# Optimization experiments

Hardware: AMD Instinct MI355X
Metric: run time of the kernel (lower is better)

## Reference

```python
import jax, jax.numpy as jnp
import numpy as np

N_NODES = 50000
N_EDGES = 600000
N_GRAPHS = 64
HID = 128
NLAYERS = 4
IN_DIM = 5
NCLS = 5
EPS = 1e-5


def setup_inputs() -> dict:
    key = jax.random.key(0)
    ks = jax.random.split(key, 16)
    x = jax.random.normal(ks[0], (N_NODES, IN_DIM), dtype=jnp.float32)
    edge_index = jax.random.randint(ks[1], (2, N_EDGES), 0, N_NODES, dtype=jnp.int64)
    batch = jnp.sort(jax.random.randint(ks[2], (N_NODES,), 0, N_GRAPHS, dtype=jnp.int64))
    s = 0.05
    Wp = jax.random.normal(ks[3], (IN_DIM, HID), jnp.float32) * s
    bp = jnp.zeros((HID,), jnp.float32)
    Wg = jax.random.normal(ks[4], (NLAYERS, HID, HID), jnp.float32) * s
    bg = jnp.zeros((NLAYERS, HID), jnp.float32)
    gamma = jnp.ones((NLAYERS, HID), jnp.float32)
    beta = jnp.zeros((NLAYERS, HID), jnp.float32)
    W1 = jax.random.normal(ks[5], (2 * HID, HID), jnp.float32) * s
    b1 = jnp.zeros((HID,), jnp.float32)
    W2 = jax.random.normal(ks[6], (HID, HID // 2), jnp.float32) * s
    b2 = jnp.zeros((HID // 2,), jnp.float32)
    W3 = jax.random.normal(ks[7], (HID // 2, NCLS), jnp.float32) * s
    b3 = jnp.zeros((NCLS,), jnp.float32)
    return {"x": x, "edge_index": edge_index, "batch": batch, "Wp": Wp, "bp": bp,
            "Wg": Wg, "bg": bg, "gamma": gamma, "beta": beta,
            "W1": W1, "b1": b1, "W2": W2, "b2": b2, "W3": W3, "b3": b3}


def reference(x, edge_index, batch, Wp, bp, Wg, bg, gamma, beta, W1, b1, W2, b2, W3, b3):
    N = x.shape[0]
    # GCN with added self-loops and symmetric normalization (PyG GCNConv defaults)
    loop = jnp.arange(N)
    src = jnp.concatenate([edge_index[0], loop])
    dst = jnp.concatenate([edge_index[1], loop])
    deg = jax.ops.segment_sum(jnp.ones_like(dst, dtype=x.dtype), dst, num_segments=N)
    dinv = jax.lax.rsqrt(deg)  # deg >= 1 thanks to self-loops
    norm = dinv[src] * dinv[dst]  # [E+N]
    h = x @ Wp + bp  # [N, HID]
    for i in range(NLAYERS):
        m = h @ Wg[i]
        agg = jax.ops.segment_sum(m[src] * norm[:, None], dst, num_segments=N) + bg[i]
        # BatchNorm1d (training-mode stats over nodes)
        mu = jnp.mean(agg, axis=0)
        var = jnp.var(agg, axis=0)
        h = gamma[i] * (agg - mu) * jax.lax.rsqrt(var + EPS) + beta[i]
        h = jax.nn.relu(h)  # dropout is identity in eval mode
    # mean_max global pooling per graph
    cnt = jax.ops.segment_sum(jnp.ones((N,), h.dtype), batch, num_segments=N_GRAPHS)
    x_mean = jax.ops.segment_sum(h, batch, num_segments=N_GRAPHS) / jnp.maximum(cnt, 1.0)[:, None]
    x_max = jax.ops.segment_max(h, batch, num_segments=N_GRAPHS)
    x_max = jnp.where(jnp.isfinite(x_max), x_max, 0.0)
    pooled = jnp.concatenate([x_mean, x_max], axis=1)  # [B, 2*HID]
    h1 = jax.nn.relu(pooled @ W1 + b1)
    h2 = jax.nn.relu(h1 @ W2 + b2)
    return h2 @ W3 + b3  # [B, num_classes]
```

## Files before the change

kernel.cpp:

```cpp
#include <hip/hip_runtime.h>
#include <hip/hip_bf16.h>

#define N_NODES 50000
#define N_EDGES 600000
#define N_GRAPHS 64
#define HID 128
#define NLAYERS 4
#define IN_DIM 5
#define NCLS 5
#define EPS 1e-5f
#define SCAN_BLK ((N_NODES + 511) / 512)
#define FILL_BLK ((N_EDGES + 255) / 256)
#define POOL_CHUNKS 16
#define BSLOT 64
#define WS 136

typedef __attribute__((ext_vector_type(8))) short s16x8;
typedef __attribute__((ext_vector_type(4))) float f32x4;

__device__ __forceinline__ unsigned short f2bf(float x) {
    unsigned u = __float_as_uint(x);
    unsigned r = (u + 0x7fffu + ((u >> 16) & 1u)) >> 16;
    return (unsigned short)r;
}
__device__ __forceinline__ float2 bfpair(unsigned u) {
    float2 r;
    r.x = __uint_as_float(u << 16);
    r.y = __uint_as_float(u & 0xffff0000u);
    return r;
}
__device__ __forceinline__ float bf2f(unsigned short s) {
    return __uint_as_float(((unsigned)s) << 16);
}


__global__ void k_count(const int* __restrict__ dst, int* __restrict__ cnt) {
    int i = blockIdx.x * blockDim.x + threadIdx.x;
    if (i < N_EDGES) atomicAdd(&cnt[dst[i]], 1);
}

__global__ void k_scan1(const int* __restrict__ cnt, int* __restrict__ rp, int* __restrict__ bsum) {
    __shared__ int s[512];
    int t = threadIdx.x;
    int i = blockIdx.x * 512 + t;
    int v = (i < N_NODES) ? cnt[i] : 0;
    s[t] = v;
    __syncthreads();
    for (int off = 1; off < 512; off <<= 1) {
        int x = (t >= off) ? s[t - off] : 0;
        __syncthreads();
        s[t] += x;
        __syncthreads();
    }
    if (i < N_NODES) rp[i + 1] = s[t];
    if (t == 511) bsum[blockIdx.x] = s[511];
}

__global__ void k_scan2g(int* __restrict__ bsum, const int* __restrict__ batch,
                         int* __restrict__ gstart) {
    if (blockIdx.x == 0) {
        __shared__ int s[128];
        int t = threadIdx.x;
        int v = (t < SCAN_BLK) ? bsum[t] : 0;
        s[t] = v;
        __syncthreads();
        for (int off = 1; off < 128; off <<= 1) {
            int x = (t >= off) ? s[t - off] : 0;
            __syncthreads();
            s[t] += x;
            __syncthreads();
        }
        if (t < SCAN_BLK) bsum[t] = s[t] - v;
    } else {
        int t = threadIdx.x;
        if (t <= N_GRAPHS) {
            int lo = 0, hi = N_NODES;
            while (lo < hi) {
                int mid = (lo + hi) >> 1;
                if (batch[mid] < t) lo = mid + 1; else hi = mid;
            }
            gstart[t] = lo;
        }
    }
}

__global__ void k_scan3d(int* __restrict__ rp, const int* __restrict__ bsum,
                         const int* __restrict__ cnt, float* __restrict__ dinv) {
    int i = blockIdx.x * 512 + threadIdx.x;
    if (i < N_NODES) {
        rp[i + 1] += bsum[blockIdx.x];
        dinv[i] = rsqrtf((float)(cnt[i] + 1));
    }
    if (i == 0) rp[0] = 0;
}

__global__ void k_fillw(const int* __restrict__ src, const int* __restrict__ dst,
                        const int* __restrict__ rp, int* __restrict__ cursor,
                        int2* __restrict__ cw, const float* __restrict__ dinv,
                        const float* __restrict__ Wg, unsigned short* __restrict__ WtG) {
    int b = blockIdx.x;
    if (b < FILL_BLK) {
        int e = b * 256 + threadIdx.x;
        if (e < N_EDGES) {
            int d = dst[e];
            int pos = atomicAdd(&cursor[d], 1);
            int s = src[e];
            int2 p;
            p.x = s;
            p.y = __float_as_int(dinv[s]);
            cw[rp[d] + pos] = p;
        }
    } else {
        int idx = (b - FILL_BLK) * 256 + threadIdx.x;
        int l = idx >> 14;
        int r = idx & 16383;
        int n = r >> 7, k = r & 127;
        WtG[idx] = f2bf(Wg[l * HID * HID + k * HID + n]);
    }
}


__global__ __launch_bounds__(256, 3) void k_gemmM(const unsigned short* __restrict__ Abf,
                                                  const float* __restrict__ x,
                                                  const float* __restrict__ Wp,
                                                  const float* __restrict__ bp,
                                                  const unsigned short* __restrict__ WtG,
                                                  unsigned short* __restrict__ Bm,
                                                  const float* __restrict__ psum,
                                                  const float* __restrict__ psq,
                                                  const float* __restrict__ gamma,
                                                  const float* __restrict__ beta,
                                                  int layer0) {
    __shared__ unsigned short Wt[HID * WS];
    __shared__ unsigned short Al[64 * WS];
    __shared__ float scl[HID], shf[HID];
    int t = threadIdx.x;
    {
        const uint4* Wg4 = (const uint4*)WtG;
        for (int idx = t; idx < HID * 16; idx += 256) {
            int n = idx >> 4, c = idx & 15;
            *(uint4*)&Wt[n * WS + c * 8] = Wg4[idx];
        }
    }
    if (!layer0 && t < HID) {
        float s = 0.f, s2 = 0.f;
#pragma unroll 8
        for (int b = 0; b < BSLOT; b++) {
            s += psum[b * HID + t];
            s2 += psq[b * HID + t];
        }
        const float invN = 1.f / (float)N_NODES;
        float mu = s * invN;
        float var = s2 * invN - mu * mu;
        float rs = rsqrtf(var + EPS) * gamma[t];
        scl[t] = rs;
        shf[t] = beta[t] - mu * rs;
    }
    int lane = t & 63, wv = t >> 6;
    int rbase = (wv & 1) * 32;
    int cbase = (wv >> 1) * 64;
    int mr = lane & 15, q = lane >> 4;
    const int numTiles = (N_NODES + 63) / 64;
    for (int tile = blockIdx.x; tile < numTiles; tile += gridDim.x) {
        int n0 = tile * 64;
        int limRow = min(64, N_NODES - n0);
        __syncthreads();
        if (layer0) {
            for (int idx = t; idx < 64 * HID; idx += 256) {
                int n = idx >> 7, k = idx & 127;
                int node = n0 + n;
                float acc = 0.f;
                if (node < N_NODES) {
                    acc = bp[k];
#pragma unroll
                    for (int j = 0; j < IN_DIM; j++) acc += x[node * IN_DIM + j] * Wp[j * HID + k];
                }
                Al[n * WS + k] = f2bf(acc);
            }
        } else {
            const uint2* Ag = (const uint2*)(Abf + (size_t)n0 * HID);
            for (int idx = t; idx < 64 * 32; idx += 256) {
                int row = idx >> 5, c4 = idx & 31;
                uint2 u = (row < limRow) ? Ag[row * 32 + c4] : make_uint2(0u, 0u);
                float2 ab = bfpair(u.x);
                float2 cd = bfpair(u.y);
                int kf = c4 * 4;
                float4 sc = *(const float4*)&scl[kf];
                float4 sh = *(const float4*)&shf[kf];
                float v0 = fmaxf(ab.x * sc.x + sh.x, 0.f);
                float v1 = fmaxf(ab.y * sc.y + sh.y, 0.f);
                float v2 = fmaxf(cd.x * sc.z + sh.z, 0.f);
                float v3 = fmaxf(cd.y * sc.w + sh.w, 0.f);
                unsigned lo = (unsigned)f2bf(v0) | ((unsigned)f2bf(v1) << 16);
                unsigned hi = (unsigned)f2bf(v2) | ((unsigned)f2bf(v3) << 16);
                *(uint2*)&Al[row * WS + kf] = make_uint2(lo, hi);
            }
        }
        __syncthreads();
        f32x4 acc[2][4];
#pragma unroll
        for (int rt = 0; rt < 2; rt++)
#pragma unroll
            for (int ct = 0; ct < 4; ct++) acc[rt][ct] = (f32x4){0.f, 0.f, 0.f, 0.f};
#pragma unroll
        for (int kk = 0; kk < HID; kk += 32) {
            s16x8 a0 = *(const s16x8*)&Al[(rbase + mr) * WS + kk + q * 8];
            s16x8 a1 = *(const s16x8*)&Al[(rbase + 16 + mr) * WS + kk + q * 8];
#pragma unroll
            for (int ct = 0; ct < 4; ct++) {
                s16x8 b = *(const s16x8*)&Wt[(cbase + ct * 16 + mr) * WS + kk + q * 8];
                acc[0][ct] = __builtin_amdgcn_mfma_f32_16x16x32_bf16(a0, b, acc[0][ct], 0, 0, 0);
                acc[1][ct] = __builtin_amdgcn_mfma_f32_16x16x32_bf16(a1, b, acc[1][ct], 0, 0, 0);
            }
        }
        __syncthreads();
#pragma unroll
        for (int rt = 0; rt < 2; rt++)
#pragma unroll
            for (int ct = 0; ct < 4; ct++)
#pragma unroll
                for (int r = 0; r < 4; r++) {
                    int rloc = rbase + rt * 16 + q * 4 + r;
                    int f = cbase + ct * 16 + mr;
                    Al[rloc * WS + f] = f2bf(acc[rt][ct][r]);
                }
        __syncthreads();
        for (int idx = t; idx < 64 * 16; idx += 256) {
            int row = idx >> 4, c = idx & 15;
            if (row < limRow)
                *(uint4*)&Bm[(size_t)(n0 + row) * HID + c * 8] = *(const uint4*)&Al[row * WS + c * 8];
        }
    }
}


__global__ __launch_bounds__(256) void k_gather(const uint4* __restrict__ Bm4,
                                                const int* __restrict__ rp,
                                                const int2* __restrict__ cw,
                                                const float* __restrict__ dinv,
                                                const float* __restrict__ bg,
                                                unsigned short* __restrict__ Aout,
                                                float* __restrict__ psum,
                                                float* __restrict__ psq) {
    __shared__ float ls[4 * HID], lq[4 * HID];
    int wave = threadIdx.x >> 6;
    int lane = threadIdx.x & 63;
    int s = lane & 15;
    int p = lane >> 4;
    int f = s * 8;
    int v = blockIdx.x * 16 + wave * 4 + p;
    int beg = rp[v], end = rp[v + 1];
    float dv = dinv[v];
    float a0, a1, a2, a3, a4, a5, a6, a7;
    {
        uint4 u = Bm4[(size_t)v * 16 + s];
        float2 q0 = bfpair(u.x), q1 = bfpair(u.y), q2 = bfpair(u.z), q3 = bfpair(u.w);
        a0 = q0.x * dv; a1 = q0.y * dv; a2 = q1.x * dv; a3 = q1.y * dv;
        a4 = q2.x * dv; a5 = q2.y * dv; a6 = q3.x * dv; a7 = q3.y * dv;
    }
    int e = beg;
    for (; e + 1 < end; e += 2) {
        int2 pe0 = cw[e];
        int2 pe1 = cw[e + 1];
        uint4 u0 = Bm4[(size_t)pe0.x * 16 + s];
        uint4 u1 = Bm4[(size_t)pe1.x * 16 + s];
        float w0 = __int_as_float(pe0.y);
        float w1 = __int_as_float(pe1.y);
        float2 x0 = bfpair(u0.x), x1 = bfpair(u0.y), x2 = bfpair(u0.z), x3 = bfpair(u0.w);
        float2 y0 = bfpair(u1.x), y1 = bfpair(u1.y), y2 = bfpair(u1.z), y3 = bfpair(u1.w);
        a0 += x0.x * w0 + y0.x * w1;
        a1 += x0.y * w0 + y0.y * w1;
        a2 += x1.x * w0 + y1.x * w1;
        a3 += x1.y * w0 + y1.y * w1;
        a4 += x2.x * w0 + y2.x * w1;
        a5 += x2.y * w0 + y2.y * w1;
        a6 += x3.x * w0 + y3.x * w1;
        a7 += x3.y * w0 + y3.y * w1;
    }
    if (e < end) {
        int2 pe = cw[e];
        uint4 u = Bm4[(size_t)pe.x * 16 + s];
        float w = __int_as_float(pe.y);
        float2 x0 = bfpair(u.x), x1 = bfpair(u.y), x2 = bfpair(u.z), x3 = bfpair(u.w);
        a0 += x0.x * w; a1 += x0.y * w; a2 += x1.x * w; a3 += x1.y * w;
        a4 += x2.x * w; a5 += x2.y * w; a6 += x3.x * w; a7 += x3.y * w;
    }
    float r0 = a0 * dv + bg[f + 0];
    float r1 = a1 * dv + bg[f + 1];
    float r2 = a2 * dv + bg[f + 2];
    float r3 = a3 * dv + bg[f + 3];
    float r4 = a4 * dv + bg[f + 4];
    float r5 = a5 * dv + bg[f + 5];
    float r6 = a6 * dv + bg[f + 6];
    float r7 = a7 * dv + bg[f + 7];
    unsigned short b0 = f2bf(r0), b1 = f2bf(r1), b2 = f2bf(r2), b3 = f2bf(r3);
    unsigned short b4 = f2bf(r4), b5 = f2bf(r5), b6 = f2bf(r6), b7 = f2bf(r7);
    uint4 o;
    o.x = (unsigned)b0 | ((unsigned)b1 << 16);
    o.y = (unsigned)b2 | ((unsigned)b3 << 16);
    o.z = (unsigned)b4 | ((unsigned)b5 << 16);
    o.w = (unsigned)b6 | ((unsigned)b7 << 16);
    *(uint4*)&Aout[(size_t)v * HID + f] = o;
    float v0 = bf2f(b0), v1 = bf2f(b1), v2 = bf2f(b2), v3 = bf2f(b3);
    float v4 = bf2f(b4), v5 = bf2f(b5), v6 = bf2f(b6), v7 = bf2f(b7);
    float ts0 = v0, ts1 = v1, ts2 = v2, ts3 = v3;
    float ts4 = v4, ts5 = v5, ts6 = v6, ts7 = v7;
    float tq0 = v0 * v0, tq1 = v1 * v1, tq2 = v2 * v2, tq3 = v3 * v3;
    float tq4 = v4 * v4, tq5 = v5 * v5, tq6 = v6 * v6, tq7 = v7 * v7;
    ts0 += __shfl_xor(ts0, 16); ts1 += __shfl_xor(ts1, 16);
    ts2 += __shfl_xor(ts2, 16); ts3 += __shfl_xor(ts3, 16);
    ts4 += __shfl_xor(ts4, 16); ts5 += __shfl_xor(ts5, 16);
    ts6 += __shfl_xor(ts6, 16); ts7 += __shfl_xor(ts7, 16);
    tq0 += __shfl_xor(tq0, 16); tq1 += __shfl_xor(tq1, 16);
    tq2 += __shfl_xor(tq2, 16); tq3 += __shfl_xor(tq3, 16);
    tq4 += __shfl_xor(tq4, 16); tq5 += __shfl_xor(tq5, 16);
    tq6 += __shfl_xor(tq6, 16); tq7 += __shfl_xor(tq7, 16);
    ts0 += __shfl_xor(ts0, 32); ts1 += __shfl_xor(ts1, 32);
    ts2 += __shfl_xor(ts2, 32); ts3 += __shfl_xor(ts3, 32);
    ts4 += __shfl_xor(ts4, 32); ts5 += __shfl_xor(ts5, 32);
    ts6 += __shfl_xor(ts6, 32); ts7 += __shfl_xor(ts7, 32);
    tq0 += __shfl_xor(tq0, 32); tq1 += __shfl_xor(tq1, 32);
    tq2 += __shfl_xor(tq2, 32); tq3 += __shfl_xor(tq3, 32);
    tq4 += __shfl_xor(tq4, 32); tq5 += __shfl_xor(tq5, 32);
    tq6 += __shfl_xor(tq6, 32); tq7 += __shfl_xor(tq7, 32);
    if (p == 0) {
        float* lsw = &ls[wave * HID + f];
        float* lqw = &lq[wave * HID + f];
        lsw[0] = ts0; lsw[1] = ts1; lsw[2] = ts2; lsw[3] = ts3;
        lsw[4] = ts4; lsw[5] = ts5; lsw[6] = ts6; lsw[7] = ts7;
        lqw[0] = tq0; lqw[1] = tq1; lqw[2] = tq2; lqw[3] = tq3;
        lqw[4] = tq4; lqw[5] = tq5; lqw[6] = tq6; lqw[7] = tq7;
    }
    __syncthreads();
    int tt = threadIdx.x;
    if (tt < HID) {
        float ssum = ls[tt] + ls[HID + tt] + ls[2 * HID + tt] + ls[3 * HID + tt];
        float ssq = lq[tt] + lq[HID + tt] + lq[2 * HID + tt] + lq[3 * HID + tt];
        int slot = blockIdx.x & (BSLOT - 1);
        atomicAdd(&psum[slot * HID + tt], ssum);
        atomicAdd(&psq[slot * HID + tt], ssq);
    }
}


__global__ __launch_bounds__(128) void k_pool(const unsigned short* __restrict__ A,
                                              const float* __restrict__ psum,
                                              const float* __restrict__ psq,
                                              const float* __restrict__ gamma,
                                              const float* __restrict__ beta,
                                              const int* __restrict__ gstart,
                                              float* __restrict__ poolPart) {
    int g = blockIdx.x;
    int c = blockIdx.y;
    int f = threadIdx.x;
    float s = 0.f, s2 = 0.f;
#pragma unroll 8
    for (int b = 0; b < BSLOT; b++) {
        s += psum[b * HID + f];
        s2 += psq[b * HID + f];
    }
    const float invN = 1.f / (float)N_NODES;
    float mu = s * invN;
    float var = s2 * invN - mu * mu;
    float sc = rsqrtf(var + EPS) * gamma[f];
    float sh = beta[f] - mu * sc;
    int beg = gstart[g], end = gstart[g + 1];
    int len = end - beg;
    int per = (len + POOL_CHUNKS - 1) / POOL_CHUNKS;
    int s0 = beg + c * per;
    int s1 = min(s0 + per, end);
    float sa = 0.f, sb = 0.f, ma = 0.f, mb = 0.f;
    int n = s0;
    for (; n + 1 < s1; n += 2) {
        float v0 = bf2f(A[(size_t)n * HID + f]);
        float v1 = bf2f(A[(size_t)(n + 1) * HID + f]);
        v0 = fmaxf(v0 * sc + sh, 0.f);
        v1 = fmaxf(v1 * sc + sh, 0.f);
        sa += v0; ma = fmaxf(ma, v0);
        sb += v1; mb = fmaxf(mb, v1);
    }
    if (n < s1) {
        float v = fmaxf(bf2f(A[(size_t)n * HID + f]) * sc + sh, 0.f);
        sa += v; ma = fmaxf(ma, v);
    }
    poolPart[((size_t)g * POOL_CHUNKS + c) * 256 + f] = sa + sb;
    poolPart[((size_t)g * POOL_CHUNKS + c) * 256 + 128 + f] = fmaxf(ma, mb);
}


__global__ __launch_bounds__(128) void k_head(const float* __restrict__ poolPart,
                                              const int* __restrict__ gstart,
                                              const float* __restrict__ W1, const float* __restrict__ b1,
                                              const float* __restrict__ W2, const float* __restrict__ b2,
                                              const float* __restrict__ W3, const float* __restrict__ b3,
                                              float* __restrict__ out) {
    __shared__ float pl[2 * HID];
    __shared__ float h1[HID];
    __shared__ float h2[HID / 2];
    int g = blockIdx.x, t = threadIdx.x;
    float cnt = fmaxf((float)(gstart[g + 1] - gstart[g]), 1.f);
    float s = 0.f, mx = 0.f;
#pragma unroll
    for (int c = 0; c < POOL_CHUNKS; c++) {
        const float* p = &poolPart[((size_t)g * POOL_CHUNKS + c) * 256];
        s += p[t];
        mx = fmaxf(mx, p[128 + t]);
    }
    pl[t] = s / cnt;
    pl[HID + t] = mx;
    __syncthreads();
    float acc = b1[t];
    for (int k = 0; k < 2 * HID; k++) acc += pl[k] * W1[k * HID + t];
    h1[t] = fmaxf(acc, 0.f);
    __syncthreads();
    if (t < HID / 2) {
        float a2 = b2[t];
        for (int k = 0; k < HID; k++) a2 += h1[k] * W2[k * (HID / 2) + t];
        h2[t] = fmaxf(a2, 0.f);
    }
    __syncthreads();
    if (t < NCLS) {
        float a3 = b3[t];
        for (int k = 0; k < HID / 2; k++) a3 += h2[k] * W3[k * NCLS + t];
        out[g * NCLS + t] = a3;
    }
}

extern "C" void kernel_launch(void* const* d_in, const int* in_sizes, int n_in,
                              void* d_out, int out_size, void* d_ws, size_t ws_size,
                              hipStream_t stream) {
    const float* x     = (const float*)d_in[0];
    const int*   ei    = (const int*)d_in[1];
    const int*   batch = (const int*)d_in[2];
    const float* Wp    = (const float*)d_in[3];
    const float* bp    = (const float*)d_in[4];
    const float* Wg    = (const float*)d_in[5];
    const float* bg    = (const float*)d_in[6];
    const float* gamma = (const float*)d_in[7];
    const float* beta  = (const float*)d_in[8];
    const float* W1    = (const float*)d_in[9];
    const float* b1    = (const float*)d_in[10];
    const float* W2    = (const float*)d_in[11];
    const float* b2    = (const float*)d_in[12];
    const float* W3    = (const float*)d_in[13];
    const float* b3    = (const float*)d_in[14];
    const int* src = ei;
    const int* dst = ei + N_EDGES;
    float* out = (float*)d_out;

    char* base = (char*)d_ws;
    size_t off = 0;
    auto alloc = [&](size_t bytes) -> void* {
        void* p = base + off;
        off += (bytes + 255) & ~(size_t)255;
        return p;
    };
    int*   counts = (int*)alloc((size_t)N_NODES * 4);
    int*   cursor = (int*)alloc((size_t)N_NODES * 4);
    float* psum   = (float*)alloc((size_t)NLAYERS * BSLOT * HID * 4);
    float* psq    = (float*)alloc((size_t)NLAYERS * BSLOT * HID * 4);
    size_t zeroBytes = off;
    int*   rp      = (int*)alloc((size_t)(N_NODES + 1) * 4);
    int*   bsum    = (int*)alloc(128 * 4);
    int2*  cw      = (int2*)alloc((size_t)N_EDGES * 8);
    float* dinv    = (float*)alloc((size_t)N_NODES * 4);
    int*   gstart  = (int*)alloc((size_t)(N_GRAPHS + 1) * 4);
    float* poolPart= (float*)alloc((size_t)N_GRAPHS * POOL_CHUNKS * 256 * 4);
    unsigned short* WtG = (unsigned short*)alloc((size_t)NLAYERS * HID * HID * 2);
    unsigned short* A = (unsigned short*)alloc((size_t)N_NODES * HID * 2);
    unsigned short* B = (unsigned short*)alloc((size_t)N_NODES * HID * 2);
    (void)ws_size; (void)in_sizes; (void)n_in; (void)out_size;

    hipMemsetAsync(d_ws, 0, zeroBytes, stream);

    k_count<<<(N_EDGES + 255) / 256, 256, 0, stream>>>(dst, counts);
    k_scan1<<<SCAN_BLK, 512, 0, stream>>>(counts, rp, bsum);
    k_scan2g<<<2, 128, 0, stream>>>(bsum, batch, gstart);
    k_scan3d<<<SCAN_BLK, 512, 0, stream>>>(rp, bsum, counts, dinv);
    k_fillw<<<FILL_BLK + (NLAYERS * HID * HID) / 256, 256, 0, stream>>>(
        src, dst, rp, cursor, cw, dinv, Wg, WtG);

    for (int i = 0; i < NLAYERS; i++) {
        int pl = (i == 0) ? 0 : (i - 1);
        k_gemmM<<<768, 256, 0, stream>>>(A, x, Wp, bp, WtG + (size_t)i * HID * HID, B,
                                         psum + (size_t)pl * BSLOT * HID,
                                         psq + (size_t)pl * BSLOT * HID,
                                         gamma + pl * HID, beta + pl * HID,
                                         (i == 0) ? 1 : 0);
        k_gather<<<N_NODES / 16, 256, 0, stream>>>((const uint4*)B, rp, cw, dinv,
                                                   bg + i * HID, A,
                                                   psum + (size_t)i * BSLOT * HID,
                                                   psq + (size_t)i * BSLOT * HID);
    }
    dim3 pg(N_GRAPHS, POOL_CHUNKS);
    k_pool<<<pg, 128, 0, stream>>>(A, psum + (size_t)3 * BSLOT * HID,
                                   psq + (size_t)3 * BSLOT * HID,
                                   gamma + 3 * HID, beta + 3 * HID, gstart, poolPart);
    k_head<<<N_GRAPHS, 128, 0, stream>>>(poolPart, gstart, W1, b1, W2, b2, W3, b3, out);
}
```

Measured before the change: 379.1 us.

## Merge graph build and all layers into two persistent cooperative kernels with grid barriers

Folds the count/scan/fill preprocessing into one cooperative kernel, and the per-layer GEMM, gather, pooling and head into a second persistent kernel. Separate launches are replaced by a software grid barrier built on atomic counters. The goal is to remove about a dozen kernel launches and their inter-kernel gaps. In exchange, every phase now runs at a fixed grid size with barrier spin overhead. The non-cooperative fallback launch relies on all blocks being co-resident, so it could deadlock.

```diff
diff --git a/kernel.cpp b/kernel.cpp
--- a/kernel.cpp
+++ b/kernel.cpp
@@ -10,10 +10,12 @@
 #define NCLS 5
 #define EPS 1e-5f
 #define SCAN_BLK ((N_NODES + 511) / 512)
-#define FILL_BLK ((N_EDGES + 255) / 256)
 #define POOL_CHUNKS 16
 #define BSLOT 64
 #define WS 136
+#define NT_BUILD (SCAN_BLK * 512)
+#define LGRID 768
+#define LGRID_FB 512
 
 typedef __attribute__((ext_vector_type(8))) short s16x8;
 typedef __attribute__((ext_vector_type(4))) float f32x4;
@@ -33,34 +35,64 @@
     return __uint_as_float(((unsigned)s) << 16);
 }
 
-
-__global__ void k_count(const int* __restrict__ dst, int* __restrict__ cnt) {
-    int i = blockIdx.x * blockDim.x + threadIdx.x;
-    if (i < N_EDGES) atomicAdd(&cnt[dst[i]], 1);
-}
-
-__global__ void k_scan1(const int* __restrict__ cnt, int* __restrict__ rp, int* __restrict__ bsum) {
+__device__ __forceinline__ void gridbar(int* cnt, int* gen, int nblk) {
+    __syncthreads();
+    if (threadIdx.x == 0) {
+        int g = __hip_atomic_load(gen, __ATOMIC_RELAXED, __HIP_MEMORY_SCOPE_AGENT);
+        __threadfence();
+        int a = __hip_atomic_fetch_add(cnt, 1, __ATOMIC_RELAXED, __HIP_MEMORY_SCOPE_AGENT);
+        if (a == nblk - 1) {
+            __hip_atomic_store(cnt, 0, __ATOMIC_RELAXED, __HIP_MEMORY_SCOPE_AGENT);
+            __hip_atomic_store(gen, g + 1, __ATOMIC_RELEASE, __HIP_MEMORY_SCOPE_AGENT);
+        } else {
+            while (__hip_atomic_load(gen, __ATOMIC_RELAXED, __HIP_MEMORY_SCOPE_AGENT) == g)
+                __builtin_amdgcn_s_sleep(2);
+        }
+        __threadfence();
+    }
+    __syncthreads();
+}
+
+
+__global__ __launch_bounds__(512) void k_build(const int* __restrict__ src,
+                                               const int* __restrict__ dst,
+                                               const int* __restrict__ batch,
+                                               const float* __restrict__ Wg,
+                                               int* __restrict__ counts,
+                                               int* __restrict__ cursor,
+                                               float* __restrict__ psum,
+                                               float* __restrict__ psq,
+                                               int* __restrict__ rp,
+                                               int* __restrict__ bsum,
+                                               int2* __restrict__ cw,
+                                               float* __restrict__ dinv,
+                                               int* __restrict__ gstart,
+                                               unsigned short* __restrict__ WtG,
+                                               int* bcnt, int* bgen) {
     __shared__ int s[512];
     int t = threadIdx.x;
-    int i = blockIdx.x * 512 + t;
-    int v = (i < N_NODES) ? cnt[i] : 0;
-    s[t] = v;
-    __syncthreads();
-    for (int off = 1; off < 512; off <<= 1) {
-        int x = (t >= off) ? s[t - off] : 0;
+    int b = blockIdx.x;
+    int gtid = b * 512 + t;
+    for (int i = gtid; i < N_NODES; i += NT_BUILD) { counts[i] = 0; cursor[i] = 0; }
+    for (int i = gtid; i < NLAYERS * BSLOT * HID; i += NT_BUILD) { psum[i] = 0.f; psq[i] = 0.f; }
+    gridbar(bcnt, bgen, SCAN_BLK);
+    for (int e = gtid; e < N_EDGES; e += NT_BUILD) atomicAdd(&counts[dst[e]], 1);
+    gridbar(bcnt, bgen, SCAN_BLK);
+    {
+        int v = (gtid < N_NODES) ? counts[gtid] : 0;
+        s[t] = v;
         __syncthreads();
-        s[t] += x;
-        __syncthreads();
-    }
-    if (i < N_NODES) rp[i + 1] = s[t];
-    if (t == 511) bsum[blockIdx.x] = s[511];
-}
-
-__global__ void k_scan2g(int* __restrict__ bsum, const int* __restrict__ batch,
-                         int* __restrict__ gstart) {
-    if (blockIdx.x == 0) {
-        __shared__ int s[128];
-        int t = threadIdx.x;
+        for (int off = 1; off < 512; off <<= 1) {
+            int x = (t >= off) ? s[t - off] : 0;
+            __syncthreads();
+            s[t] += x;
+            __syncthreads();
+        }
+        if (gtid < N_NODES) rp[gtid + 1] = s[t];
+        if (t == 511) bsum[b] = s[511];
+    }
+    gridbar(bcnt, bgen, SCAN_BLK);
+    if (b == 0) {
         int v = (t < SCAN_BLK) ? bsum[t] : 0;
         s[t] = v;
         __syncthreads();
@@ -71,8 +103,7 @@
             __syncthreads();
         }
         if (t < SCAN_BLK) bsum[t] = s[t] - v;
-    } else {
-        int t = threadIdx.x;
+    } else if (b == 1) {
         if (t <= N_GRAPHS) {
             int lo = 0, hi = N_NODES;
             while (lo < hi) {
@@ -82,36 +113,23 @@
             gstart[t] = lo;
         }
     }
-}
-
-__global__ void k_scan3d(int* __restrict__ rp, const int* __restrict__ bsum,
-                         const int* __restrict__ cnt, float* __restrict__ dinv) {
-    int i = blockIdx.x * 512 + threadIdx.x;
-    if (i < N_NODES) {
-        rp[i + 1] += bsum[blockIdx.x];
-        dinv[i] = rsqrtf((float)(cnt[i] + 1));
-    }
-    if (i == 0) rp[0] = 0;
-}
-
-__global__ void k_fillw(const int* __restrict__ src, const int* __restrict__ dst,
-                        const int* __restrict__ rp, int* __restrict__ cursor,
-                        int2* __restrict__ cw, const float* __restrict__ dinv,
-                        const float* __restrict__ Wg, unsigned short* __restrict__ WtG) {
-    int b = blockIdx.x;
-    if (b < FILL_BLK) {
-        int e = b * 256 + threadIdx.x;
-        if (e < N_EDGES) {
-            int d = dst[e];
-            int pos = atomicAdd(&cursor[d], 1);
-            int s = src[e];
-            int2 p;
-            p.x = s;
-            p.y = __float_as_int(dinv[s]);
-            cw[rp[d] + pos] = p;
-        }
-    } else {
-        int idx = (b - FILL_BLK) * 256 + threadIdx.x;
+    gridbar(bcnt, bgen, SCAN_BLK);
+    if (gtid < N_NODES) {
+        rp[gtid + 1] += bsum[b];
+        dinv[gtid] = rsqrtf((float)(counts[gtid] + 1));
+    }
+    if (gtid == 0) rp[0] = 0;
+    gridbar(bcnt, bgen, SCAN_BLK);
+    for (int e = gtid; e < N_EDGES; e += NT_BUILD) {
+        int d = dst[e];
+        int pos = atomicAdd(&cursor[d], 1);
+        int sn = src[e];
+        int2 p;
+        p.x = sn;
+        p.y = __float_as_int(dinv[sn]);
+        cw[rp[d] + pos] = p;
+    }
+    for (int idx = gtid; idx < NLAYERS * HID * HID; idx += NT_BUILD) {
         int l = idx >> 14;
         int r = idx & 16383;
         int n = r >> 7, k = r & 127;
@@ -120,309 +138,325 @@
 }
 
 
-__global__ __launch_bounds__(256, 3) void k_gemmM(const unsigned short* __restrict__ Abf,
-                                                  const float* __restrict__ x,
-                                                  const float* __restrict__ Wp,
-                                                  const float* __restrict__ bp,
-                                                  const unsigned short* __restrict__ WtG,
-                                                  unsigned short* __restrict__ Bm,
-                                                  const float* __restrict__ psum,
-                                                  const float* __restrict__ psq,
-                                                  const float* __restrict__ gamma,
-                                                  const float* __restrict__ beta,
-                                                  int layer0) {
+__global__ __launch_bounds__(256, 3) void k_layers(const float* __restrict__ x,
+                                                   const float* __restrict__ Wp,
+                                                   const float* __restrict__ bp,
+                                                   const unsigned short* __restrict__ WtG,
+                                                   const float* __restrict__ bgA,
+                                                   const float* __restrict__ gammaA,
+                                                   const float* __restrict__ betaA,
+                                                   const int* __restrict__ rp,
+                                                   const int2* __restrict__ cw,
+                                                   const float* __restrict__ dinv,
+                                                   const int* __restrict__ gstart,
+                                                   unsigned short* __restrict__ A,
+                                                   unsigned short* __restrict__ B,
+                                                   float* __restrict__ psumA,
+                                                   float* __restrict__ psqA,
+                                                   const float* __restrict__ W1,
+                                                   const float* __restrict__ b1,
+                                                   const float* __restrict__ W2,
+                                                   const float* __restrict__ b2,
+                                                   const float* __restrict__ W3,
+                                                   const float* __restrict__ b3,
+                                                   float* __restrict__ out,
+                                                   float* __restrict__ poolPart,
+                                                   int* bcnt, int* bgen) {
     __shared__ unsigned short Wt[HID * WS];
     __shared__ unsigned short Al[64 * WS];
     __shared__ float scl[HID], shf[HID];
     int t = threadIdx.x;
+    int nblk = gridDim.x;
+    int lane = t & 63, wv = t >> 6;
+
+    for (int l = 0; l < NLAYERS; l++) {
+        const unsigned short* Wl = WtG + (size_t)l * HID * HID;
+        int pl = (l == 0) ? 0 : (l - 1);
+        const float* psum = psumA + (size_t)pl * BSLOT * HID;
+        const float* psq = psqA + (size_t)pl * BSLOT * HID;
+        {
+            const uint4* Wg4 = (const uint4*)Wl;
+            for (int idx = t; idx < HID * 16; idx += 256) {
+                int n = idx >> 4, c = idx & 15;
+                *(uint4*)&Wt[n * WS + c * 8] = Wg4[idx];
+            }
+        }
+        if (l > 0 && t < HID) {
+            float s = 0.f, s2 = 0.f;
+#pragma unroll 8
+            for (int bb = 0; bb < BSLOT; bb++) {
+                s += psum[bb * HID + t];
+                s2 += psq[bb * HID + t];
+            }
+            const float invN = 1.f / (float)N_NODES;
+            float mu = s * invN;
+            float var = s2 * invN - mu * mu;
+            float rs = rsqrtf(var + EPS) * gammaA[pl * HID + t];
+            scl[t] = rs;
+            shf[t] = betaA[pl * HID + t] - mu * rs;
+        }
+        int rbase = (wv & 1) * 32;
+        int cbase = (wv >> 1) * 64;
+        int mr = lane & 15, q = lane >> 4;
+        const int numTiles = (N_NODES + 63) / 64;
+        for (int tile = blockIdx.x; tile < numTiles; tile += nblk) {
+            int n0 = tile * 64;
+            int limRow = min(64, N_NODES - n0);
+            __syncthreads();
+            if (l == 0) {
+                for (int idx = t; idx < 64 * HID; idx += 256) {
+                    int n = idx >> 7, k = idx & 127;
+                    int node = n0 + n;
+                    float acc = 0.f;
+                    if (node < N_NODES) {
+                        acc = bp[k];
+#pragma unroll
+                        for (int j = 0; j < IN_DIM; j++) acc += x[node * IN_DIM + j] * Wp[j * HID + k];
+                    }
+                    Al[n * WS + k] = f2bf(acc);
+                }
+            } else {
+                const uint2* Ag = (const uint2*)(A + (size_t)n0 * HID);
+                for (int idx = t; idx < 64 * 32; idx += 256) {
+                    int row = idx >> 5, c4 = idx & 31;
+                    uint2 u = (row < limRow) ? Ag[row * 32 + c4] : make_uint2(0u, 0u);
+                    float2 ab = bfpair(u.x);
+                    float2 cd = bfpair(u.y);
+                    int kf = c4 * 4;
+                    float4 sc = *(const float4*)&scl[kf];
+                    float4 sh = *(const float4*)&shf[kf];
+                    float v0 = fmaxf(ab.x * sc.x + sh.x, 0.f);
+                    float v1 = fmaxf(ab.y * sc.y + sh.y, 0.f);
+                    float v2 = fmaxf(cd.x * sc.z + sh.z, 0.f);
+                    float v3 = fmaxf(cd.y * sc.w + sh.w, 0.f);
+                    unsigned lo = (unsigned)f2bf(v0) | ((unsigned)f2bf(v1) << 16);
+                    unsigned hi = (unsigned)f2bf(v2) | ((unsigned)f2bf(v3) << 16);
+                    *(uint2*)&Al[row * WS + kf] = make_uint2(lo, hi);
+                }
+            }
+            __syncthreads();
+            f32x4 acc[2][4];
+#pragma unroll
+            for (int rt = 0; rt < 2; rt++)
+#pragma unroll
+                for (int ct = 0; ct < 4; ct++) acc[rt][ct] = (f32x4){0.f, 0.f, 0.f, 0.f};
+#pragma unroll
+            for (int kk = 0; kk < HID; kk += 32) {
+                s16x8 a0 = *(const s16x8*)&Al[(rbase + mr) * WS + kk + q * 8];
+                s16x8 a1 = *(const s16x8*)&Al[(rbase + 16 + mr) * WS + kk + q * 8];
+#pragma unroll
+                for (int ct = 0; ct < 4; ct++) {
+                    s16x8 bfr = *(const s16x8*)&Wt[(cbase + ct * 16 + mr) * WS + kk + q * 8];
+                    acc[0][ct] = __builtin_amdgcn_mfma_f32_16x16x32_bf16(a0, bfr, acc[0][ct], 0, 0, 0);
+                    acc[1][ct] = __builtin_amdgcn_mfma_f32_16x16x32_bf16(a1, bfr, acc[1][ct], 0, 0, 0);
+                }
+            }
+            __syncthreads();
+#pragma unroll
+            for (int rt = 0; rt < 2; rt++)
+#pragma unroll
+                for (int ct = 0; ct < 4; ct++)
+#pragma unroll
+                    for (int r = 0; r < 4; r++) {
+                        int rloc = rbase + rt * 16 + q * 4 + r;
+                        int f = cbase + ct * 16 + mr;
+                        Al[rloc * WS + f] = f2bf(acc[rt][ct][r]);
+                    }
+            __syncthreads();
+            for (int idx = t; idx < 64 * 16; idx += 256) {
+                int row = idx >> 4, c = idx & 15;
+                if (row < limRow)
+                    *(uint4*)&B[(size_t)(n0 + row) * HID + c * 8] = *(const uint4*)&Al[row * WS + c * 8];
+            }
+        }
+        gridbar(bcnt, bgen, nblk);
+
+        {
+            const uint4* Bm4 = (const uint4*)B;
+            float* ls = (float*)Wt;
+            float* lq = ls + 4 * HID;
+            const float* bgl = bgA + l * HID;
+            float* psumW = psumA + (size_t)l * BSLOT * HID;
+            float* psqW = psqA + (size_t)l * BSLOT * HID;
+            int sfc = lane & 15;
+            int p = lane >> 4;
+            int f = sfc * 8;
+            for (int u = blockIdx.x; u < N_NODES / 16; u += nblk) {
+                int v = u * 16 + wv * 4 + p;
+                int beg = rp[v], end = rp[v + 1];
+                float dv = dinv[v];
+                float a0, a1, a2, a3, a4, a5, a6, a7;
+                {
+                    uint4 uu = Bm4[(size_t)v * 16 + sfc];
+                    float2 q0 = bfpair(uu.x), q1 = bfpair(uu.y), q2 = bfpair(uu.z), q3 = bfpair(uu.w);
+                    a0 = q0.x * dv; a1 = q0.y * dv; a2 = q1.x * dv; a3 = q1.y * dv;
+                    a4 = q2.x * dv; a5 = q2.y * dv; a6 = q3.x * dv; a7 = q3.y * dv;
+                }
+                int e = beg;
+                for (; e + 1 < end; e += 2) {
+                    int2 pe0 = cw[e];
+                    int2 pe1 = cw[e + 1];
+                    uint4 u0 = Bm4[(size_t)pe0.x * 16 + sfc];
+                    uint4 u1 = Bm4[(size_t)pe1.x * 16 + sfc];
+                    float w0 = __int_as_float(pe0.y);
+                    float w1 = __int_as_float(pe1.y);
+                    float2 x0 = bfpair(u0.x), x1 = bfpair(u0.y), x2 = bfpair(u0.z), x3 = bfpair(u0.w);
+                    float2 y0 = bfpair(u1.x), y1 = bfpair(u1.y), y2 = bfpair(u1.z), y3 = bfpair(u1.w);
+                    a0 += x0.x * w0 + y0.x * w1;
+                    a1 += x0.y * w0 + y0.y * w1;
+                    a2 += x1.x * w0 + y1.x * w1;
+                    a3 += x1.y * w0 + y1.y * w1;
+                    a4 += x2.x * w0 + y2.x * w1;
+                    a5 += x2.y * w0 + y2.y * w1;
+                    a6 += x3.x * w0 + y3.x * w1;
+                    a7 += x3.y * w0 + y3.y * w1;
+                }
+                if (e < end) {
+                    int2 pe = cw[e];
+                    uint4 uu = Bm4[(size_t)pe.x * 16 + sfc];
+                    float w = __int_as_float(pe.y);
+                    float2 x0 = bfpair(uu.x), x1 = bfpair(uu.y), x2 = bfpair(uu.z), x3 = bfpair(uu.w);
+                    a0 += x0.x * w; a1 += x0.y * w; a2 += x1.x * w; a3 += x1.y * w;
+                    a4 += x2.x * w; a5 += x2.y * w; a6 += x3.x * w; a7 += x3.y * w;
+                }
+                float r0 = a0 * dv + bgl[f + 0];
+                float r1 = a1 * dv + bgl[f + 1];
+                float r2 = a2 * dv + bgl[f + 2];
+                float r3 = a3 * dv + bgl[f + 3];
+                float r4 = a4 * dv + bgl[f + 4];
+                float r5 = a5 * dv + bgl[f + 5];
+                float r6 = a6 * dv + bgl[f + 6];
+                float r7 = a7 * dv + bgl[f + 7];
+                unsigned short c0 = f2bf(r0), c1 = f2bf(r1), c2 = f2bf(r2), c3 = f2bf(r3);
+                unsigned short c4 = f2bf(r4), c5 = f2bf(r5), c6 = f2bf(r6), c7 = f2bf(r7);
+                uint4 o;
+                o.x = (unsigned)c0 | ((unsigned)c1 << 16);
+                o.y = (unsigned)c2 | ((unsigned)c3 << 16);
+                o.z = (unsigned)c4 | ((unsigned)c5 << 16);
+                o.w = (unsigned)c6 | ((unsigned)c7 << 16);
+                *(uint4*)&A[(size_t)v * HID + f] = o;
+                float v0 = bf2f(c0), v1 = bf2f(c1), v2 = bf2f(c2), v3 = bf2f(c3);
+                float v4 = bf2f(c4), v5 = bf2f(c5), v6 = bf2f(c6), v7 = bf2f(c7);
+                float ts0 = v0, ts1 = v1, ts2 = v2, ts3 = v3;
+                float ts4 = v4, ts5 = v5, ts6 = v6, ts7 = v7;
+                float tq0 = v0 * v0, tq1 = v1 * v1, tq2 = v2 * v2, tq3 = v3 * v3;
+                float tq4 = v4 * v4, tq5 = v5 * v5, tq6 = v6 * v6, tq7 = v7 * v7;
+                ts0 += __shfl_xor(ts0, 16); ts1 += __shfl_xor(ts1, 16);
+                ts2 += __shfl_xor(ts2, 16); ts3 += __shfl_xor(ts3, 16);
+                ts4 += __shfl_xor(ts4, 16); ts5 += __shfl_xor(ts5, 16);
+                ts6 += __shfl_xor(ts6, 16); ts7 += __shfl_xor(ts7, 16);
+                tq0 += __shfl_xor(tq0, 16); tq1 += __shfl_xor(tq1, 16);
+                tq2 += __shfl_xor(tq2, 16); tq3 += __shfl_xor(tq3, 16);
+                tq4 += __shfl_xor(tq4, 16); tq5 += __shfl_xor(tq5, 16);
+                tq6 += __shfl_xor(tq6, 16); tq7 += __shfl_xor(tq7, 16);
+                ts0 += __shfl_xor(ts0, 32); ts1 += __shfl_xor(ts1, 32);
+                ts2 += __shfl_xor(ts2, 32); ts3 += __shfl_xor(ts3, 32);
+                ts4 += __shfl_xor(ts4, 32); ts5 += __shfl_xor(ts5, 32);
+                ts6 += __shfl_xor(ts6, 32); ts7 += __shfl_xor(ts7, 32);
+                tq0 += __shfl_xor(tq0, 32); tq1 += __shfl_xor(tq1, 32);
+                tq2 += __shfl_xor(tq2, 32); tq3 += __shfl_xor(tq3, 32);
+                tq4 += __shfl_xor(tq4, 32); tq5 += __shfl_xor(tq5, 32);
+                tq6 += __shfl_xor(tq6, 32); tq7 += __shfl_xor(tq7, 32);
+                if (p == 0) {
+                    float* lsw = &ls[wv * HID + f];
+                    float* lqw = &lq[wv * HID + f];
+                    lsw[0] = ts0; lsw[1] = ts1; lsw[2] = ts2; lsw[3] = ts3;
+                    lsw[4] = ts4; lsw[5] = ts5; lsw[6] = ts6; lsw[7] = ts7;
+                    lqw[0] = tq0; lqw[1] = tq1; lqw[2] = tq2; lqw[3] = tq3;
+                    lqw[4] = tq4; lqw[5] = tq5; lqw[6] = tq6; lqw[7] = tq7;
+                }
+                __syncthreads();
+                if (t < HID) {
+                    float ssum = ls[t] + ls[HID + t] + ls[2 * HID + t] + ls[3 * HID + t];
+                    float ssq = lq[t] + lq[HID + t] + lq[2 * HID + t] + lq[3 * HID + t];
+                    int slot = u & (BSLOT - 1);
+                    atomicAdd(&psumW[slot * HID + t], ssum);
+                    atomicAdd(&psqW[slot * HID + t], ssq);
+                }
+                __syncthreads();
+            }
+        }
+        gridbar(bcnt, bgen, nblk);
+    }
+
     {
-        const uint4* Wg4 = (const uint4*)WtG;
-        for (int idx = t; idx < HID * 16; idx += 256) {
-            int n = idx >> 4, c = idx & 15;
-            *(uint4*)&Wt[n * WS + c * 8] = Wg4[idx];
-        }
-    }
-    if (!layer0 && t < HID) {
-        float s = 0.f, s2 = 0.f;
+        const float* psum3 = psumA + (size_t)3 * BSLOT * HID;
+        const float* psq3 = psqA + (size_t)3 * BSLOT * HID;
+        int half = t >> 7;
+        int f = t & 127;
+        for (int u = blockIdx.x * 2 + half; u < N_GRAPHS * POOL_CHUNKS; u += nblk * 2) {
+            int g = u >> 4, c = u & (POOL_CHUNKS - 1);
+            float s = 0.f, s2 = 0.f;
 #pragma unroll 8
-        for (int b = 0; b < BSLOT; b++) {
-            s += psum[b * HID + t];
-            s2 += psq[b * HID + t];
-        }
-        const float invN = 1.f / (float)N_NODES;
-        float mu = s * invN;
-        float var = s2 * invN - mu * mu;
-        float rs = rsqrtf(var + EPS) * gamma[t];
-        scl[t] = rs;
-        shf[t] = beta[t] - mu * rs;
-    }
-    int lane = t & 63, wv = t >> 6;
-    int rbase = (wv & 1) * 32;
-    int cbase = (wv >> 1) * 64;
-    int mr = lane & 15, q = lane >> 4;
-    const int numTiles = (N_NODES + 63) / 64;
-    for (int tile = blockIdx.x; tile < numTiles; tile += gridDim.x) {
-        int n0 = tile * 64;
-        int limRow = min(64, N_NODES - n0);
+            for (int bb = 0; bb < BSLOT; bb++) {
+                s += psum3[bb * HID + f];
+                s2 += psq3[bb * HID + f];
+            }
+            const float invN = 1.f / (float)N_NODES;
+            float mu = s * invN;
+            float var = s2 * invN - mu * mu;
+            float sc = rsqrtf(var + EPS) * gammaA[3 * HID + f];
+            float sh = betaA[3 * HID + f] - mu * sc;
+            int beg = gstart[g], end = gstart[g + 1];
+            int len = end - beg;
+            int per = (len + POOL_CHUNKS - 1) / POOL_CHUNKS;
+            int s0 = beg + c * per;
+            int s1 = min(s0 + per, end);
+            float sa = 0.f, sb = 0.f, ma = 0.f, mb = 0.f;
+            int n = s0;
+            for (; n + 1 < s1; n += 2) {
+                float v0 = bf2f(A[(size_t)n * HID + f]);
+                float v1 = bf2f(A[(size_t)(n + 1) * HID + f]);
+                v0 = fmaxf(v0 * sc + sh, 0.f);
+                v1 = fmaxf(v1 * sc + sh, 0.f);
+                sa += v0; ma = fmaxf(ma, v0);
+                sb += v1; mb = fmaxf(mb, v1);
+            }
+            if (n < s1) {
+                float v = fmaxf(bf2f(A[(size_t)n * HID + f]) * sc + sh, 0.f);
+                sa += v; ma = fmaxf(ma, v);
+            }
+            poolPart[((size_t)g * POOL_CHUNKS + c) * 256 + f] = sa + sb;
+            poolPart[((size_t)g * POOL_CHUNKS + c) * 256 + 128 + f] = fmaxf(ma, mb);
+        }
+    }
+    gridbar(bcnt, bgen, nblk);
+
+    if (blockIdx.x < N_GRAPHS) {
+        float* plm = (float*)Al;
+        float* h1 = plm + 2 * HID;
+        float* h2 = h1 + HID;
+        int g = blockIdx.x;
+        float gcnt = fmaxf((float)(gstart[g + 1] - gstart[g]), 1.f);
+        if (t < 128) {
+            float s = 0.f, mx = 0.f;
+#pragma unroll
+            for (int c = 0; c < POOL_CHUNKS; c++) {
+                const float* pp = &poolPart[((size_t)g * POOL_CHUNKS + c) * 256];
+                s += pp[t];
+                mx = fmaxf(mx, pp[128 + t]);
+            }
+            plm[t] = s / gcnt;
+            plm[HID + t] = mx;
+        }
         __syncthreads();
-        if (layer0) {
-            for (int idx = t; idx < 64 * HID; idx += 256) {
-                int n = idx >> 7, k = idx & 127;
-                int node = n0 + n;
-                float acc = 0.f;
-                if (node < N_NODES) {
-                    acc = bp[k];
-#pragma unroll
-                    for (int j = 0; j < IN_DIM; j++) acc += x[node * IN_DIM + j] * Wp[j * HID + k];
-                }
-                Al[n * WS + k] = f2bf(acc);
-            }
-        } else {
-            const uint2* Ag = (const uint2*)(Abf + (size_t)n0 * HID);
-            for (int idx = t; idx < 64 * 32; idx += 256) {
-                int row = idx >> 5, c4 = idx & 31;
-                uint2 u = (row < limRow) ? Ag[row * 32 + c4] : make_uint2(0u, 0u);
-                float2 ab = bfpair(u.x);
-                float2 cd = bfpair(u.y);
-                int kf = c4 * 4;
-                float4 sc = *(const float4*)&scl[kf];
-                float4 sh = *(const float4*)&shf[kf];
-                float v0 = fmaxf(ab.x * sc.x + sh.x, 0.f);
-                float v1 = fmaxf(ab.y * sc.y + sh.y, 0.f);
-                float v2 = fmaxf(cd.x * sc.z + sh.z, 0.f);
-                float v3 = fmaxf(cd.y * sc.w + sh.w, 0.f);
-                unsigned lo = (unsigned)f2bf(v0) | ((unsigned)f2bf(v1) << 16);
-                unsigned hi = (unsigned)f2bf(v2) | ((unsigned)f2bf(v3) << 16);
-                *(uint2*)&Al[row * WS + kf] = make_uint2(lo, hi);
-            }
+        if (t < 128) {
+            float acc = b1[t];
+            for (int k = 0; k < 2 * HID; k++) acc += plm[k] * W1[k * HID + t];
+            h1[t] = fmaxf(acc, 0.f);
         }
         __syncthreads();
-        f32x4 acc[2][4];
-#pragma unroll
-        for (int rt = 0; rt < 2; rt++)
-#pragma unroll
-            for (int ct = 0; ct < 4; ct++) acc[rt][ct] = (f32x4){0.f, 0.f, 0.f, 0.f};
-#pragma unroll
-        for (int kk = 0; kk < HID; kk += 32) {
-            s16x8 a0 = *(const s16x8*)&Al[(rbase + mr) * WS + kk + q * 8];
-            s16x8 a1 = *(const s16x8*)&Al[(rbase + 16 + mr) * WS + kk + q * 8];
-#pragma unroll
-            for (int ct = 0; ct < 4; ct++) {
-                s16x8 b = *(const s16x8*)&Wt[(cbase + ct * 16 + mr) * WS + kk + q * 8];
-                acc[0][ct] = __builtin_amdgcn_mfma_f32_16x16x32_bf16(a0, b, acc[0][ct], 0, 0, 0);
-                acc[1][ct] = __builtin_amdgcn_mfma_f32_16x16x32_bf16(a1, b, acc[1][ct], 0, 0, 0);
-            }
+        if (t < HID / 2) {
+            float a2 = b2[t];
+            for (int k = 0; k < HID; k++) a2 += h1[k] * W2[k * (HID / 2) + t];
+            h2[t] = fmaxf(a2, 0.f);
         }
         __syncthreads();
-#pragma unroll
-        for (int rt = 0; rt < 2; rt++)
-#pragma unroll
-            for (int ct = 0; ct < 4; ct++)
-#pragma unroll
-                for (int r = 0; r < 4; r++) {
-                    int rloc = rbase + rt * 16 + q * 4 + r;
-                    int f = cbase + ct * 16 + mr;
-                    Al[rloc * WS + f] = f2bf(acc[rt][ct][r]);
-                }
-        __syncthreads();
-        for (int idx = t; idx < 64 * 16; idx += 256) {
-            int row = idx >> 4, c = idx & 15;
-            if (row < limRow)
-                *(uint4*)&Bm[(size_t)(n0 + row) * HID + c * 8] = *(const uint4*)&Al[row * WS + c * 8];
-        }
-    }
-}
-
-
-__global__ __launch_bounds__(256) void k_gather(const uint4* __restrict__ Bm4,
-                                                const int* __restrict__ rp,
-                                                const int2* __restrict__ cw,
-                                                const float* __restrict__ dinv,
-                                                const float* __restrict__ bg,
-                                                unsigned short* __restrict__ Aout,
-                                                float* __restrict__ psum,
-                                                float* __restrict__ psq) {
-    __shared__ float ls[4 * HID], lq[4 * HID];
-    int wave = threadIdx.x >> 6;
-    int lane = threadIdx.x & 63;
-    int s = lane & 15;
-    int p = lane >> 4;
-    int f = s * 8;
-    int v = blockIdx.x * 16 + wave * 4 + p;
-    int beg = rp[v], end = rp[v + 1];
-    float dv = dinv[v];
-    float a0, a1, a2, a3, a4, a5, a6, a7;
-    {
-        uint4 u = Bm4[(size_t)v * 16 + s];
-        float2 q0 = bfpair(u.x), q1 = bfpair(u.y), q2 = bfpair(u.z), q3 = bfpair(u.w);
-        a0 = q0.x * dv; a1 = q0.y * dv; a2 = q1.x * dv; a3 = q1.y * dv;
-        a4 = q2.x * dv; a5 = q2.y * dv; a6 = q3.x * dv; a7 = q3.y * dv;
-    }
-    int e = beg;
-    for (; e + 1 < end; e += 2) {
-        int2 pe0 = cw[e];
-        int2 pe1 = cw[e + 1];
-        uint4 u0 = Bm4[(size_t)pe0.x * 16 + s];
-        uint4 u1 = Bm4[(size_t)pe1.x * 16 + s];
-        float w0 = __int_as_float(pe0.y);
-        float w1 = __int_as_float(pe1.y);
-        float2 x0 = bfpair(u0.x), x1 = bfpair(u0.y), x2 = bfpair(u0.z), x3 = bfpair(u0.w);
-        float2 y0 = bfpair(u1.x), y1 = bfpair(u1.y), y2 = bfpair(u1.z), y3 = bfpair(u1.w);
-        a0 += x0.x * w0 + y0.x * w1;
-        a1 += x0.y * w0 + y0.y * w1;
-        a2 += x1.x * w0 + y1.x * w1;
-        a3 += x1.y * w0 + y1.y * w1;
-        a4 += x2.x * w0 + y2.x * w1;
-        a5 += x2.y * w0 + y2.y * w1;
-        a6 += x3.x * w0 + y3.x * w1;
-        a7 += x3.y * w0 + y3.y * w1;
-    }
-    if (e < end) {
-        int2 pe = cw[e];
-        uint4 u = Bm4[(size_t)pe.x * 16 + s];
-        float w = __int_as_float(pe.y);
-        float2 x0 = bfpair(u.x), x1 = bfpair(u.y), x2 = bfpair(u.z), x3 = bfpair(u.w);
-        a0 += x0.x * w; a1 += x0.y * w; a2 += x1.x * w; a3 += x1.y * w;
-        a4 += x2.x * w; a5 += x2.y * w; a6 += x3.x * w; a7 += x3.y * w;
-    }
-    float r0 = a0 * dv + bg[f + 0];
-    float r1 = a1 * dv + bg[f + 1];
-    float r2 = a2 * dv + bg[f + 2];
-    float r3 = a3 * dv + bg[f + 3];
-    float r4 = a4 * dv + bg[f + 4];
-    float r5 = a5 * dv + bg[f + 5];
-    float r6 = a6 * dv + bg[f + 6];
-    float r7 = a7 * dv + bg[f + 7];
-    unsigned short b0 = f2bf(r0), b1 = f2bf(r1), b2 = f2bf(r2), b3 = f2bf(r3);
-    unsigned short b4 = f2bf(r4), b5 = f2bf(r5), b6 = f2bf(r6), b7 = f2bf(r7);
-    uint4 o;
-    o.x = (unsigned)b0 | ((unsigned)b1 << 16);
-    o.y = (unsigned)b2 | ((unsigned)b3 << 16);
-    o.z = (unsigned)b4 | ((unsigned)b5 << 16);
-    o.w = (unsigned)b6 | ((unsigned)b7 << 16);
-    *(uint4*)&Aout[(size_t)v * HID + f] = o;
-    float v0 = bf2f(b0), v1 = bf2f(b1), v2 = bf2f(b2), v3 = bf2f(b3);
-    float v4 = bf2f(b4), v5 = bf2f(b5), v6 = bf2f(b6), v7 = bf2f(b7);
-    float ts0 = v0, ts1 = v1, ts2 = v2, ts3 = v3;
-    float ts4 = v4, ts5 = v5, ts6 = v6, ts7 = v7;
-    float tq0 = v0 * v0, tq1 = v1 * v1, tq2 = v2 * v2, tq3 = v3 * v3;
-    float tq4 = v4 * v4, tq5 = v5 * v5, tq6 = v6 * v6, tq7 = v7 * v7;
-    ts0 += __shfl_xor(ts0, 16); ts1 += __shfl_xor(ts1, 16);
-    ts2 += __shfl_xor(ts2, 16); ts3 += __shfl_xor(ts3, 16);
-    ts4 += __shfl_xor(ts4, 16); ts5 += __shfl_xor(ts5, 16);
-    ts6 += __shfl_xor(ts6, 16); ts7 += __shfl_xor(ts7, 16);
-    tq0 += __shfl_xor(tq0, 16); tq1 += __shfl_xor(tq1, 16);
-    tq2 += __shfl_xor(tq2, 16); tq3 += __shfl_xor(tq3, 16);
-    tq4 += __shfl_xor(tq4, 16); tq5 += __shfl_xor(tq5, 16);
-    tq6 += __shfl_xor(tq6, 16); tq7 += __shfl_xor(tq7, 16);
-    ts0 += __shfl_xor(ts0, 32); ts1 += __shfl_xor(ts1, 32);
-    ts2 += __shfl_xor(ts2, 32); ts3 += __shfl_xor(ts3, 32);
-    ts4 += __shfl_xor(ts4, 32); ts5 += __shfl_xor(ts5, 32);
-    ts6 += __shfl_xor(ts6, 32); ts7 += __shfl_xor(ts7, 32);
-    tq0 += __shfl_xor(tq0, 32); tq1 += __shfl_xor(tq1, 32);
-    tq2 += __shfl_xor(tq2, 32); tq3 += __shfl_xor(tq3, 32);
-    tq4 += __shfl_xor(tq4, 32); tq5 += __shfl_xor(tq5, 32);
-    tq6 += __shfl_xor(tq6, 32); tq7 += __shfl_xor(tq7, 32);
-    if (p == 0) {
-        float* lsw = &ls[wave * HID + f];
-        float* lqw = &lq[wave * HID + f];
-        lsw[0] = ts0; lsw[1] = ts1; lsw[2] = ts2; lsw[3] = ts3;
-        lsw[4] = ts4; lsw[5] = ts5; lsw[6] = ts6; lsw[7] = ts7;
-        lqw[0] = tq0; lqw[1] = tq1; lqw[2] = tq2; lqw[3] = tq3;
-        lqw[4] = tq4; lqw[5] = tq5; lqw[6] = tq6; lqw[7] = tq7;
-    }
-    __syncthreads();
-    int tt = threadIdx.x;
-    if (tt < HID) {
-        float ssum = ls[tt] + ls[HID + tt] + ls[2 * HID + tt] + ls[3 * HID + tt];
-        float ssq = lq[tt] + lq[HID + tt] + lq[2 * HID + tt] + lq[3 * HID + tt];
-        int slot = blockIdx.x & (BSLOT - 1);
-        atomicAdd(&psum[slot * HID + tt], ssum);
-        atomicAdd(&psq[slot * HID + tt], ssq);
-    }
-}
-
-
-__global__ __launch_bounds__(128) void k_pool(const unsigned short* __restrict__ A,
-                                              const float* __restrict__ psum,
-                                              const float* __restrict__ psq,
-                                              const float* __restrict__ gamma,
-                                              const float* __restrict__ beta,
-                                              const int* __restrict__ gstart,
-                                              float* __restrict__ poolPart) {
-    int g = blockIdx.x;
-    int c = blockIdx.y;
-    int f = threadIdx.x;
-    float s = 0.f, s2 = 0.f;
-#pragma unroll 8
-    for (int b = 0; b < BSLOT; b++) {
-        s += psum[b * HID + f];
-        s2 += psq[b * HID + f];
-    }
-    const float invN = 1.f / (float)N_NODES;
-    float mu = s * invN;
-    float var = s2 * invN - mu * mu;
-    float sc = rsqrtf(var + EPS) * gamma[f];
-    float sh = beta[f] - mu * sc;
-    int beg = gstart[g], end = gstart[g + 1];
-    int len = end - beg;
-    int per = (len + POOL_CHUNKS - 1) / POOL_CHUNKS;
-    int s0 = beg + c * per;
-    int s1 = min(s0 + per, end);
-    float sa = 0.f, sb = 0.f, ma = 0.f, mb = 0.f;
-    int n = s0;
-    for (; n + 1 < s1; n += 2) {
-        float v0 = bf2f(A[(size_t)n * HID + f]);
-        float v1 = bf2f(A[(size_t)(n + 1) * HID + f]);
-        v0 = fmaxf(v0 * sc + sh, 0.f);
-        v1 = fmaxf(v1 * sc + sh, 0.f);
-        sa += v0; ma = fmaxf(ma, v0);
-        sb += v1; mb = fmaxf(mb, v1);
-    }
-    if (n < s1) {
-        float v = fmaxf(bf2f(A[(size_t)n * HID + f]) * sc + sh, 0.f);
-        sa += v; ma = fmaxf(ma, v);
-    }
-    poolPart[((size_t)g * POOL_CHUNKS + c) * 256 + f] = sa + sb;
-    poolPart[((size_t)g * POOL_CHUNKS + c) * 256 + 128 + f] = fmaxf(ma, mb);
-}
-
-
-__global__ __launch_bounds__(128) void k_head(const float* __restrict__ poolPart,
-                                              const int* __restrict__ gstart,
-                                              const float* __restrict__ W1, const float* __restrict__ b1,
-                                              const float* __restrict__ W2, const float* __restrict__ b2,
-                                              const float* __restrict__ W3, const float* __restrict__ b3,
-                                              float* __restrict__ out) {
-    __shared__ float pl[2 * HID];
-    __shared__ float h1[HID];
-    __shared__ float h2[HID / 2];
-    int g = blockIdx.x, t = threadIdx.x;
-    float cnt = fmaxf((float)(gstart[g + 1] - gstart[g]), 1.f);
-    float s = 0.f, mx = 0.f;
-#pragma unroll
-    for (int c = 0; c < POOL_CHUNKS; c++) {
-        const float* p = &poolPart[((size_t)g * POOL_CHUNKS + c) * 256];
-        s += p[t];
-        mx = fmaxf(mx, p[128 + t]);
-    }
-    pl[t] = s / cnt;
-    pl[HID + t] = mx;
-    __syncthreads();
-    float acc = b1[t];
-    for (int k = 0; k < 2 * HID; k++) acc += pl[k] * W1[k * HID + t];
-    h1[t] = fmaxf(acc, 0.f);
-    __syncthreads();
-    if (t < HID / 2) {
-        float a2 = b2[t];
-        for (int k = 0; k < HID; k++) a2 += h1[k] * W2[k * (HID / 2) + t];
-        h2[t] = fmaxf(a2, 0.f);
-    }
-    __syncthreads();
-    if (t < NCLS) {
-        float a3 = b3[t];
-        for (int k = 0; k < HID / 2; k++) a3 += h2[k] * W3[k * NCLS + t];
-        out[g * NCLS + t] = a3;
+        if (t < NCLS) {
+            float a3 = b3[t];
+            for (int k = 0; k < HID / 2; k++) a3 += h2[k] * W3[k * NCLS + t];
+            out[g * NCLS + t] = a3;
+        }
     }
 }
 
@@ -455,11 +489,13 @@
         off += (bytes + 255) & ~(size_t)255;
         return p;
     };
+    int* bcnt = (int*)alloc(4);
+    int* bgen = (int*)alloc(4);
+    size_t zeroBytes = off;
     int*   counts = (int*)alloc((size_t)N_NODES * 4);
     int*   cursor = (int*)alloc((size_t)N_NODES * 4);
     float* psum   = (float*)alloc((size_t)NLAYERS * BSLOT * HID * 4);
     float* psq    = (float*)alloc((size_t)NLAYERS * BSLOT * HID * 4);
-    size_t zeroBytes = off;
     int*   rp      = (int*)alloc((size_t)(N_NODES + 1) * 4);
     int*   bsum    = (int*)alloc(128 * 4);
     int2*  cw      = (int2*)alloc((size_t)N_EDGES * 8);
@@ -473,28 +509,31 @@
 
     hipMemsetAsync(d_ws, 0, zeroBytes, stream);
 
-    k_count<<<(N_EDGES + 255) / 256, 256, 0, stream>>>(dst, counts);
-    k_scan1<<<SCAN_BLK, 512, 0, stream>>>(counts, rp, bsum);
-    k_scan2g<<<2, 128, 0, stream>>>(bsum, batch, gstart);
-    k_scan3d<<<SCAN_BLK, 512, 0, stream>>>(rp, bsum, counts, dinv);
-    k_fillw<<<FILL_BLK + (NLAYERS * HID * HID) / 256, 256, 0, stream>>>(
-        src, dst, rp, cursor, cw, dinv, Wg, WtG);
-
-    for (int i = 0; i < NLAYERS; i++) {
-        int pl = (i == 0) ? 0 : (i - 1);
-        k_gemmM<<<768, 256, 0, stream>>>(A, x, Wp, bp, WtG + (size_t)i * HID * HID, B,
-                                         psum + (size_t)pl * BSLOT * HID,
-                                         psq + (size_t)pl * BSLOT * HID,
-                                         gamma + pl * HID, beta + pl * HID,
-                                         (i == 0) ? 1 : 0);
-        k_gather<<<N_NODES / 16, 256, 0, stream>>>((const uint4*)B, rp, cw, dinv,
-                                                   bg + i * HID, A,
-                                                   psum + (size_t)i * BSLOT * HID,
-                                                   psq + (size_t)i * BSLOT * HID);
-    }
-    dim3 pg(N_GRAPHS, POOL_CHUNKS);
-    k_pool<<<pg, 128, 0, stream>>>(A, psum + (size_t)3 * BSLOT * HID,
-                                   psq + (size_t)3 * BSLOT * HID,
-                                   gamma + 3 * HID, beta + 3 * HID, gstart, poolPart);
-    k_head<<<N_GRAPHS, 128, 0, stream>>>(poolPart, gstart, W1, b1, W2, b2, W3, b3, out);
-}
+    {
+        void* bargs[] = { (void*)&src, (void*)&dst, (void*)&batch, (void*)&Wg,
+                          (void*)&counts, (void*)&cursor, (void*)&psum, (void*)&psq,
+                          (void*)&rp, (void*)&bsum, (void*)&cw, (void*)&dinv,
+                          (void*)&gstart, (void*)&WtG, (void*)&bcnt, (void*)&bgen };
+        if (hipLaunchCooperativeKernel((void*)k_build, dim3(SCAN_BLK), dim3(512),
+                                       bargs, 0, stream) != hipSuccess) {
+            k_build<<<SCAN_BLK, 512, 0, stream>>>(src, dst, batch, Wg, counts, cursor,
+                                                  psum, psq, rp, bsum, cw, dinv, gstart,
+                                                  WtG, bcnt, bgen);
+        }
+    }
+    {
+        void* largs[] = { (void*)&x, (void*)&Wp, (void*)&bp, (void*)&WtG, (void*)&bg,
+                          (void*)&gamma, (void*)&beta, (void*)&rp, (void*)&cw,
+                          (void*)&dinv, (void*)&gstart, (void*)&A, (void*)&B,
+                          (void*)&psum, (void*)&psq, (void*)&W1, (void*)&b1,
+                          (void*)&W2, (void*)&b2, (void*)&W3, (void*)&b3,
+                          (void*)&out, (void*)&poolPart, (void*)&bcnt, (void*)&bgen };
+        if (hipLaunchCooperativeKernel((void*)k_layers, dim3(LGRID), dim3(256),
+                                       largs, 0, stream) != hipSuccess) {
+            k_layers<<<LGRID_FB, 256, 0, stream>>>(x, Wp, bp, WtG, bg, gamma, beta, rp,
+                                                   cw, dinv, gstart, A, B, psum, psq,
+                                                   W1, b1, W2, b2, W3, b3, out, poolPart,
+                                                   bcnt, bgen);
+        }
+    }
+}
```

After: 801.1 us. 2.11x slower.
